# Kernel tuning notes

Measured on AMD Instinct MI355X. Metric: run time of the kernel, lower is better.

The kernel has to match this reference:

```python
import jax, jax.numpy as jnp
import numpy as np

DIM = 192
HEADS = 6
WS = (2, 7, 7)
SHIFT = (1, 3, 3)
MLP_HID = int(DIM * 4.0)
N = WS[0] * WS[1] * WS[2]  # 98


def _relative_position_index():
    wt, wh, ww = WS
    coords = np.stack(np.meshgrid(np.arange(wt), np.arange(wh), np.arange(ww), indexing='ij'))
    cf = coords.reshape(3, -1)  # (3, N)
    rel = cf[:, :, None] - cf[:, None, :]  # (3, N, N)
    rel = rel.transpose(1, 2, 0).copy()
    rel[:, :, 0] += wt - 1
    rel[:, :, 1] += wh - 1
    rel[:, :, 2] += ww - 1
    rel[:, :, 0] *= (2 * wh - 1) * (2 * ww - 1)
    rel[:, :, 1] *= 2 * ww - 1
    return rel.sum(-1)  # (N, N) int

RPI = jnp.asarray(_relative_position_index())


def setup_inputs() -> dict:
    key = jax.random.key(0)
    ks = jax.random.split(key, 12)
    B, C, T, H, W = 2, DIM, 8, 56, 56
    n_bias = (2 * WS[0] - 1) * (2 * WS[1] - 1) * (2 * WS[2] - 1)
    s = lambda k, shp, sd=0.02: jax.random.normal(k, shp, jnp.float32) * sd
    return {
        'x': jax.random.normal(ks[0], (B, C, T, H, W), jnp.float32),
        'mask_matrix': jnp.zeros((256, N, N), jnp.float32),
        'norm1_g': jnp.ones((DIM,), jnp.float32),
        'norm1_b': jnp.zeros((DIM,), jnp.float32),
        'qkv_w': s(ks[1], (DIM, 3 * DIM)),
        'qkv_b': jnp.zeros((3 * DIM,), jnp.float32),
        'proj_w': s(ks[2], (DIM, DIM)),
        'proj_b': jnp.zeros((DIM,), jnp.float32),
        'rpb_table': s(ks[3], (n_bias, HEADS)),
        'norm2_g': jnp.ones((DIM,), jnp.float32),
        'norm2_b': jnp.zeros((DIM,), jnp.float32),
        'fc1_w': s(ks[4], (DIM, MLP_HID)),
        'fc1_b': jnp.zeros((MLP_HID,), jnp.float32),
        'fc2_w': s(ks[5], (MLP_HID, DIM)),
        'fc2_b': jnp.zeros((DIM,), jnp.float32),
    }


def _layernorm(x, g, b, eps=1e-5):
    mu = jnp.mean(x, -1, keepdims=True)
    var = jnp.var(x, -1, keepdims=True)
    return (x - mu) * jax.lax.rsqrt(var + eps) * g + b


def _window_partition(x):
    # x: (B, T, H, W, C) -> (B*nW, N, C)
    B, T, H, W, C = x.shape
    wt, wh, ww = WS
    x = x.reshape(B, T // wt, wt, H // wh, wh, W // ww, ww, C)
    x = x.transpose(0, 1, 3, 5, 2, 4, 6, 7)
    return x.reshape(-1, wt * wh * ww, C)


def _window_reverse(win, B, T, H, W):
    wt, wh, ww = WS
    C = win.shape[-1]
    x = win.reshape(B, T // wt, H // wh, W // ww, wt, wh, ww, C)
    x = x.transpose(0, 1, 4, 2, 5, 3, 6, 7)
    return x.reshape(B, T, H, W, C)


def reference(x, mask_matrix, norm1_g, norm1_b, qkv_w, qkv_b, proj_w, proj_b,
              rpb_table, norm2_g, norm2_b, fc1_w, fc1_b, fc2_w, fc2_b):
    B, C, T, H, W = x.shape
    hd = C // HEADS
    scale = hd ** -0.5

    shortcut = x.transpose(0, 2, 3, 4, 1)  # (B,T,H,W,C) channel-last residual
    xn = _layernorm(shortcut, norm1_g, norm1_b)
    # cyclic shift
    xs = jnp.roll(xn, shift=(-SHIFT[0], -SHIFT[1], -SHIFT[2]), axis=(1, 2, 3))
    xw = _window_partition(xs)  # (B_, N, C)
    B_ = xw.shape[0]

    qkv = (xw @ qkv_w + qkv_b).reshape(B_, N, 3, HEADS, hd)
    q, k, v = (qkv[:, :, 0].transpose(0, 2, 1, 3),
               qkv[:, :, 1].transpose(0, 2, 1, 3),
               qkv[:, :, 2].transpose(0, 2, 1, 3))  # (B_, h, N, d)
    attn = jnp.einsum('bhnd,bhmd->bhnm', q * scale, k)
    bias = rpb_table[RPI.reshape(-1)].reshape(N, N, HEADS).transpose(2, 0, 1)
    attn = attn + bias[None]
    nW = mask_matrix.shape[0]
    attn = attn.reshape(B_ // nW, nW, HEADS, N, N) + mask_matrix[None, :, None]
    attn = jax.nn.softmax(attn.reshape(B_, HEADS, N, N), axis=-1)
    out = jnp.einsum('bhnm,bhmd->bhnd', attn, v).transpose(0, 2, 1, 3).reshape(B_, N, C)
    out = out @ proj_w + proj_b

    xr = _window_reverse(out, B, T, H, W)
    xr = jnp.roll(xr, shift=SHIFT, axis=(1, 2, 3))
    x1 = shortcut + xr

    xn2 = _layernorm(x1, norm2_g, norm2_b)
    h1 = jax.nn.gelu(xn2 @ fc1_w + fc1_b, approximate=False)
    x2 = x1 + (h1 @ fc2_w + fc2_b)
    return x2.transpose(0, 4, 1, 2, 3)  # (B, C, T, H, W)
```

## Files before the change

kernel.cpp:

```cpp
#include <hip/hip_runtime.h>
#include <hip/hip_bf16.h>
#include <math.h>

#define DEV __device__ __forceinline__

typedef __bf16 bf16;
typedef __bf16 bf16x8 __attribute__((ext_vector_type(8)));
typedef float f32x4 __attribute__((ext_vector_type(4)));

DEV f32x4 zero4() { f32x4 z; z[0]=0.f; z[1]=0.f; z[2]=0.f; z[3]=0.f; return z; }

DEV void gload_lds16(const bf16* g, bf16* l) {
    __builtin_amdgcn_global_load_lds(
        (const __attribute__((address_space(1))) void*)g,
        (__attribute__((address_space(3))) void*)l, 16, 0, 0);
}

DEV float gelu_f(float v) {
    float z = 0.7978845608028654f * (v + 0.044715f * v * v * v);
    float e = __expf(-2.0f * fabsf(z));
    float t = __builtin_copysignf((1.0f - e) / (1.0f + e), z);
    return 0.5f * v * (1.0f + t);
}


__global__ __launch_bounds__(256) void prep_w_k(
    const float* __restrict__ qw, const float* __restrict__ pw,
    const float* __restrict__ f1, const float* __restrict__ f2,
    bf16* __restrict__ qwt, bf16* __restrict__ pwt,
    bf16* __restrict__ f1t, bf16* __restrict__ f2t)
{
    int i = blockIdx.x * 256 + threadIdx.x;
    if (i < 576*192) { int n = i / 192, k = i % 192; qwt[i] = (bf16)qw[(size_t)k*576 + n]; }
    if (i < 192*192) { int n = i / 192, k = i % 192; pwt[i] = (bf16)pw[(size_t)k*192 + n]; }
    if (i < 768*192) { int n = i / 192, k = i % 192; f1t[i] = (bf16)f1[(size_t)k*768 + n]; }
    if (i < 192*768) { int n = i / 768, k = i % 768; f2t[i] = (bf16)f2[(size_t)k*192 + n]; }
}

__global__ __launch_bounds__(256) void prep_biasF_k(
    const float* __restrict__ rpb, float* __restrict__ biasF)
{
    int i = blockIdx.x * 256 + threadIdx.x;
    if (i >= 6*7*7*64) return;
    int lane = i & 63; int g = i >> 6;
    int j = g % 7; g /= 7; int rt = g % 7; int head = g / 7;
    int l15 = lane & 15, lg = lane >> 4;
    int nk = j*16 + l15;
    f32x4 o;
    #pragma unroll
    for (int r = 0; r < 4; r++) {
        int nq = rt*16 + lg*4 + r; if (nq > 97) nq = 97;
        if (nk < 98) {
            int t1 = nq/49, r1 = nq%49, h1 = r1/7, w1 = r1%7;
            int t2 = nk/49, r2 = nk%49, h2 = r2/7, w2 = r2%7;
            int idx = (t1 - t2 + 1)*169 + (h1 - h2 + 6)*13 + (w1 - w2 + 6);
            o[r] = rpb[idx*6 + head];
        } else {
            o[r] = -1e30f;
        }
    }
    *(f32x4*)&biasF[(size_t)i*4] = o;
}

__global__ __launch_bounds__(256) void prep_maskF_k(
    const float* __restrict__ maskm, float* __restrict__ maskF)
{
    int i = blockIdx.x * 256 + threadIdx.x;
    if (i >= 256*7*7*64) return;
    int lane = i & 63; int g = i >> 6;
    int j = g % 7; g /= 7; int rt = g % 7; int wib = g / 7;
    int l15 = lane & 15, lg = lane >> 4;
    int nk = j*16 + l15;
    f32x4 o;
    #pragma unroll
    for (int r = 0; r < 4; r++) {
        int nq = rt*16 + lg*4 + r; if (nq > 97) nq = 97;
        o[r] = (nk < 98) ? maskm[((size_t)wib*98 + nq)*98 + nk] : 0.f;
    }
    *(f32x4*)&maskF[(size_t)i*4] = o;
}

__global__ __launch_bounds__(256) void ln1_window_k(
    const float* __restrict__ x, const float* __restrict__ g,
    const float* __restrict__ bta, bf16* __restrict__ xw)
{
    __shared__ float tile[56*193];
    __shared__ float mu[56], rs[56];
    int blk = blockIdx.x;
    int bb = blk / 448; int r = blk % 448; int ts = r / 56; int hs = r % 56;
    int t = (ts + 1) & 7;
    int h = hs + 3; if (h >= 56) h -= 56;
    int tid = threadIdx.x;
    const float* xs = x + ((size_t)bb*1536 + t)*3136 + h*56;
    for (int e = tid; e < 192*56; e += 256) {
        int c = e / 56, w = e % 56;
        int wsp = w - 3; if (wsp < 0) wsp += 56;
        tile[wsp*193 + c] = xs[(size_t)c*25088 + w];
    }
    __syncthreads();
    if (tid < 224) {
        int row = tid >> 2, q = tid & 3;
        float s = 0.f, s2 = 0.f;
        for (int c = q*48; c < q*48 + 48; c++) {
            float v = tile[row*193 + c]; s += v; s2 += v*v;
        }
        s  += __shfl_xor(s, 1);  s  += __shfl_xor(s, 2);
        s2 += __shfl_xor(s2, 1); s2 += __shfl_xor(s2, 2);
        if (q == 0) {
            float m = s * (1.0f/192.0f);
            mu[row] = m;
            rs[row] = rsqrtf(s2 * (1.0f/192.0f) - m*m + 1e-5f);
        }
    }
    __syncthreads();
    int tb = ts >> 1, wt = ts & 1;
    int hb = hs / 7, wh = hs % 7;
    for (int e = tid; e < 56*192; e += 256) {
        int wpos = e / 192, c = e % 192;
        float v = (tile[wpos*193 + c] - mu[wpos]) * rs[wpos] * g[c] + bta[c];
        int wb = wpos / 7, ww = wpos % 7;
        int widx = bb*256 + tb*64 + hb*8 + wb;
        int n = wt*49 + wh*7 + ww;
        xw[((size_t)widx*98 + n)*192 + c] = (bf16)v;
    }
}

template<int KT, int NT, int BN, int EPI>
__global__ __launch_bounds__(256) void gemm_k(
    const bf16* __restrict__ A, const bf16* __restrict__ BT,
    const float* __restrict__ bias, const float* __restrict__ resid,
    void* __restrict__ outp)
{
    __shared__ bf16 la[2][128*64];
    __shared__ bf16 lb[2][BN*64];
    constexpr int NTILES = NT / BN;
    constexpr int NK = KT / 64;
    constexpr int JT = BN / 32;
    constexpr int WN = BN / 2;
    constexpr int SPX = 392 / 8;
    int blk = blockIdx.x;
    int xcd = blk & 7, ix = blk >> 3;
    int m0 = (xcd * SPX + ix / NTILES) * 128;
    int n0 = (ix % NTILES) * BN;
    int tid = threadIdx.x;
    int lane = tid & 63;
    int wv = tid >> 6;
    int wr = wv >> 1, wc = wv & 1;
    int l15 = lane & 15, lg = lane >> 4;

    auto stage = [&](int kt, int buf) {
        int kb = kt * 64;
        #pragma unroll
        for (int t = 0; t < 4; t++) {
            int e = t*256 + wv*64 + lane;
            int row = e >> 3, ck = e & 7;
            gload_lds16(&A[(size_t)(m0 + row)*KT + kb + ((ck ^ (row & 7)) << 3)],
                        &la[buf][(t*256 + wv*64) * 8]);
        }
        #pragma unroll
        for (int t = 0; t < JT; t++) {
            int e = t*256 + wv*64 + lane;
            int row = e >> 3, ck = e & 7;
            gload_lds16(&BT[(size_t)(n0 + row)*KT + kb + ((ck ^ (row & 7)) << 3)],
                        &lb[buf][(t*256 + wv*64) * 8]);
        }
    };

    f32x4 acc[4][JT];
    #pragma unroll
    for (int i = 0; i < 4; i++)
        #pragma unroll
        for (int j = 0; j < JT; j++) acc[i][j] = zero4();

    stage(0, 0);
    __syncthreads();

    for (int kt = 0; kt < NK; kt++) {
        int cur = kt & 1;
        if (kt + 1 < NK) stage(kt + 1, cur ^ 1);
        const bf16* lab = la[cur];
        const bf16* lbb = lb[cur];
        #pragma unroll
        for (int ks = 0; ks < 64; ks += 32) {
            int lc = (ks >> 3) + lg;
            bf16x8 af[4], bfr[JT];
            #pragma unroll
            for (int i = 0; i < 4; i++) {
                int ri = wr*64 + i*16 + l15;
                af[i] = *(const bf16x8*)&lab[ri*64 + ((lc ^ (ri & 7)) << 3)];
            }
            #pragma unroll
            for (int j = 0; j < JT; j++) {
                int rj = wc*WN + j*16 + l15;
                bfr[j] = *(const bf16x8*)&lbb[rj*64 + ((lc ^ (rj & 7)) << 3)];
            }
            #pragma unroll
            for (int i = 0; i < 4; i++)
                #pragma unroll
                for (int j = 0; j < JT; j++)
                    acc[i][j] = __builtin_amdgcn_mfma_f32_16x16x32_bf16(af[i], bfr[j], acc[i][j], 0, 0, 0);
        }
        __syncthreads();
    }

    if constexpr (EPI == 4) {
        #pragma unroll
        for (int i = 0; i < 4; i++) {
            #pragma unroll
            for (int j = 0; j < JT; j++) {
                int row0 = m0 + wr*64 + i*16 + lg*4;
                int col = n0 + wc*WN + j*16 + l15;
                f32x4 o;
                #pragma unroll
                for (int r = 0; r < 4; r++)
                    o[r] = acc[i][j][r] + bias[col] + resid[(size_t)(row0 + r)*NT + col];
                int bb2 = row0 >= 25088;
                size_t off = (size_t)bb2*192*25088 + (size_t)col*25088 + (row0 - bb2*25088);
                *(f32x4*)&((float*)outp)[off] = o;
            }
        }
    } else {
        #pragma unroll
        for (int i = 0; i < 4; i++) {
            #pragma unroll
            for (int j = 0; j < JT; j++) {
                #pragma unroll
                for (int r = 0; r < 4; r++) {
                    int row = m0 + wr*64 + i*16 + lg*4 + r;
                    int col = n0 + wc*WN + j*16 + l15;
                    float v = acc[i][j][r] + bias[col];
                    size_t oidx = (size_t)row * NT + col;
                    if constexpr (EPI == 0) {
                        ((bf16*)outp)[oidx] = (bf16)v;
                    } else if constexpr (EPI == 1) {
                        ((float*)outp)[oidx] = v;
                    } else if constexpr (EPI == 2) {
                        ((bf16*)outp)[oidx] = (bf16)gelu_f(v);
                    }
                }
            }
        }
    }
}

__global__ __launch_bounds__(128) void attn_k(
    const bf16* __restrict__ qkv, const float* __restrict__ biasF,
    const float* __restrict__ maskF, bf16* __restrict__ aout)
{
    __shared__ bf16 VT[32*128];
    __shared__ bf16 Pl[2*16*136];
    int blk = blockIdx.x;
    int t8 = (blk & 7) * 384 + (blk >> 3);
    int b_ = t8 / 6, head = t8 % 6;
    int tid = threadIdx.x, lane = tid & 63, wv = tid >> 6;
    int l15 = lane & 15, lg = (lane >> 4) & 3;
    int wib = b_ & 255;
    const bf16* base = qkv + (size_t)b_*98*576;

    {
        unsigned int* vz = (unsigned int*)VT;
        for (int e = tid; e < 2048; e += 128) vz[e] = 0u;
        unsigned int* pz = (unsigned int*)Pl;
        for (int e = tid; e < 256; e += 128) {
            int w2 = e >> 7, rem = e & 127;
            int row = rem >> 3, cp = rem & 7;
            pz[(w2*16 + row)*68 + 56 + cp] = 0u;
        }
    }
    __syncthreads();
    {
        int dq = tid >> 5;
        int kl = tid & 31;
        const bf16* vbase = base + 384 + head*32 + dq*8;
        #pragma unroll
        for (int kr = 0; kr < 4; kr++) {
            int k = kr*32 + kl;
            if (k < 98) {
                bf16x8 v8 = *(const bf16x8*)&vbase[(size_t)k*576];
                #pragma unroll
                for (int j = 0; j < 8; j++)
                    VT[(dq*8 + j)*128 + (k ^ (j << 3))] = v8[j];
            }
        }
    }
    __syncthreads();

    bf16x8 kfr[7];
    #pragma unroll
    for (int j = 0; j < 7; j++) {
        int krow = j*16 + l15; if (krow > 97) krow = 97;
        kfr[j] = *(const bf16x8*)&base[(size_t)krow*576 + 192 + head*32 + lg*8];
    }

    const float scale = 0.17677669529663687f;
    bf16* Pw = Pl + wv*16*136;
    const int rt0 = wv ? 4 : 0, rt1 = wv ? 7 : 4;

    auto loadQ = [&](int rt) {
        int qrow = rt*16 + l15; if (qrow > 97) qrow = 97;
        return *(const bf16x8*)&base[(size_t)qrow*576 + head*32 + lg*8];
    };
    bf16x8 qf = loadQ(rt0);

    #pragma unroll 1
    for (int rt = rt0; rt < rt1; rt++) {
        bf16x8 qnext = qf;
        if (rt + 1 < rt1) qnext = loadQ(rt + 1);
        f32x4 sacc[7];
        #pragma unroll
        for (int j = 0; j < 7; j++) sacc[j] = zero4();
        #pragma unroll
        for (int j = 0; j < 7; j++)
            sacc[j] = __builtin_amdgcn_mfma_f32_16x16x32_bf16(qf, kfr[j], sacc[j], 0, 0, 0);
        {
            const float* bfp = biasF + ((size_t)(head*7 + rt)*7)*256 + lane*4;
            const float* mfp = maskF + ((size_t)(wib*7 + rt)*7)*256 + lane*4;
            #pragma unroll
            for (int j = 0; j < 7; j++) {
                f32x4 bv = *(const f32x4*)&bfp[j*256];
                f32x4 mv = *(const f32x4*)&mfp[j*256];
                sacc[j] = sacc[j]*scale + bv + mv;
            }
            f32x4 m4 = sacc[0];
            #pragma unroll
            for (int j = 1; j < 7; j++) {
                #pragma unroll
                for (int r = 0; r < 4; r++) m4[r] = fmaxf(m4[r], sacc[j][r]);
            }
            #pragma unroll
            for (int d = 1; d < 16; d <<= 1) {
                #pragma unroll
                for (int r = 0; r < 4; r++) m4[r] = fmaxf(m4[r], __shfl_xor(m4[r], d));
            }
            f32x4 s4 = zero4();
            #pragma unroll
            for (int j = 0; j < 7; j++) {
                #pragma unroll
                for (int r = 0; r < 4; r++) sacc[j][r] = __expf(sacc[j][r] - m4[r]);
                s4 += sacc[j];
            }
            #pragma unroll
            for (int d = 1; d < 16; d <<= 1) {
                #pragma unroll
                for (int r = 0; r < 4; r++) s4[r] += __shfl_xor(s4[r], d);
            }
            f32x4 inv4;
            #pragma unroll
            for (int r = 0; r < 4; r++) inv4[r] = 1.0f / s4[r];
            #pragma unroll
            for (int j = 0; j < 7; j++)
                #pragma unroll
                for (int r = 0; r < 4; r++)
                    Pw[(lg*4 + r)*136 + j*16 + l15] = (bf16)(sacc[j][r]*inv4[r]);
        }
        #pragma unroll
        for (int dt = 0; dt < 2; dt++) {
            int dl = dt*16 + l15;
            int xr = (dl & 7) << 3;
            f32x4 oacc = zero4();
            #pragma unroll
            for (int kc = 0; kc < 4; kc++) {
                bf16x8 pf = *(const bf16x8*)&Pw[l15*136 + kc*32 + lg*8];
                bf16x8 vf = *(const bf16x8*)&VT[dl*128 + ((kc*32 + lg*8) ^ xr)];
                oacc = __builtin_amdgcn_mfma_f32_16x16x32_bf16(pf, vf, oacc, 0, 0, 0);
            }
            #pragma unroll
            for (int r = 0; r < 4; r++) {
                int row = rt*16 + lg*4 + r;
                if (row < 98)
                    aout[((size_t)b_*98 + row)*192 + head*32 + dt*16 + l15] = (bf16)oacc[r];
            }
        }
        qf = qnext;
    }
}

__global__ __launch_bounds__(256) void rev_res_ln2_k(
    const float* __restrict__ x, const float* __restrict__ pw,
    const float* __restrict__ g2, const float* __restrict__ b2,
    float* __restrict__ x1, bf16* __restrict__ xn2)
{
    __shared__ float tile[56*193];
    __shared__ float mu[56], rs[56];
    int blk = blockIdx.x;
    int bb = blk / 448; int r = blk % 448; int t = r / 56; int h = r % 56;
    int ts = (t + 7) & 7;
    int hs = h - 3; if (hs < 0) hs += 56;
    int tid = threadIdx.x;
    const float* xs = x + ((size_t)bb*1536 + t)*3136 + h*56;
    for (int e = tid; e < 192*56; e += 256) {
        int c = e / 56, w = e % 56;
        tile[w*193 + c] = xs[(size_t)c*25088 + w];
    }
    __syncthreads();
    int tb = ts >> 1, wt = ts & 1, hb = hs / 7, wh = hs % 7;
    for (int e = tid; e < 56*192; e += 256) {
        int w = e / 192, c = e % 192;
        int wsp = w - 3; if (wsp < 0) wsp += 56;
        int wb = wsp / 7, ww = wsp % 7;
        size_t tok = (size_t)(bb*256 + tb*64 + hb*8 + wb)*98 + wt*49 + wh*7 + ww;
        tile[w*193 + c] += pw[tok*192 + c];
    }
    __syncthreads();
    if (tid < 224) {
        int row = tid >> 2, q = tid & 3;
        float s = 0.f, s2 = 0.f;
        for (int c = q*48; c < q*48 + 48; c++) {
            float v = tile[row*193 + c]; s += v; s2 += v*v;
        }
        s  += __shfl_xor(s, 1);  s  += __shfl_xor(s, 2);
        s2 += __shfl_xor(s2, 1); s2 += __shfl_xor(s2, 2);
        if (q == 0) {
            float m = s * (1.0f/192.0f);
            mu[row] = m;
            rs[row] = rsqrtf(s2 * (1.0f/192.0f) - m*m + 1e-5f);
        }
    }
    __syncthreads();
    size_t tok0 = ((size_t)(bb*8 + t)*56 + h)*56;
    for (int e = tid; e < 56*192; e += 256) {
        int w = e / 192, c = e % 192;
        float v = tile[w*193 + c];
        x1[(tok0 + w)*192 + c] = v;
        xn2[(tok0 + w)*192 + c] = (bf16)((v - mu[w]) * rs[w] * g2[c] + b2[c]);
    }
}

extern "C" void kernel_launch(void* const* d_in, const int* in_sizes, int n_in,
                              void* d_out, int out_size, void* d_ws, size_t ws_size,
                              hipStream_t stream)
{
    const float* x     = (const float*)d_in[0];
    const float* maskm = (const float*)d_in[1];
    const float* n1g   = (const float*)d_in[2];
    const float* n1b   = (const float*)d_in[3];
    const float* qkvw  = (const float*)d_in[4];
    const float* qkvb  = (const float*)d_in[5];
    const float* projw = (const float*)d_in[6];
    const float* projb = (const float*)d_in[7];
    const float* rpb   = (const float*)d_in[8];
    const float* n2g   = (const float*)d_in[9];
    const float* n2b   = (const float*)d_in[10];
    const float* f1w   = (const float*)d_in[11];
    const float* f1b   = (const float*)d_in[12];
    const float* f2w   = (const float*)d_in[13];
    const float* f2b   = (const float*)d_in[14];

    char* ws = (char*)d_ws;
    bf16*  qkv_wt  = (bf16*)(ws + 0);
    bf16*  proj_wt = (bf16*)(ws + 221184);
    bf16*  fc1_wt  = (bf16*)(ws + 294912);
    bf16*  fc2_wt  = (bf16*)(ws + 589824);
    float* biasF   = (float*)(ws + 884736);
    bf16* xw   = (bf16*)(ws + 1179648);
    bf16* aout = xw;
    char* Bp = ws + 1179648 + 19267584;
    bf16*  qkv  = (bf16*)Bp;
    float* pwin = (float*)Bp;
    char* Cp = Bp + 57802752;
    float* x1  = (float*)Cp;
    bf16*  xn2 = (bf16*)(Cp + 38535168);
    bf16*  h1  = (bf16*)(Cp + 38535168 + 19267584);
    float* maskF = (float*)(Cp + 38535168 + 19267584);

    prep_w_k<<<576, 256, 0, stream>>>(qkvw, projw, f1w, f2w, qkv_wt, proj_wt, fc1_wt, fc2_wt);
    prep_biasF_k<<<74, 256, 0, stream>>>(rpb, biasF);
    prep_maskF_k<<<3136, 256, 0, stream>>>(maskm, maskF);
    ln1_window_k<<<896, 256, 0, stream>>>(x, n1g, n1b, xw);
    gemm_k<192, 576, 192, 0><<<392*3, 256, 0, stream>>>(xw, qkv_wt, qkvb, nullptr, qkv);
    attn_k<<<3072, 128, 0, stream>>>(qkv, biasF, maskF, aout);
    gemm_k<192, 192, 64, 1><<<392*3, 256, 0, stream>>>(aout, proj_wt, projb, nullptr, pwin);
    rev_res_ln2_k<<<896, 256, 0, stream>>>(x, pwin, n2g, n2b, x1, xn2);
    gemm_k<192, 768, 64, 2><<<392*12, 256, 0, stream>>>(xn2, fc1_wt, f1b, nullptr, h1);
    gemm_k<768, 192, 64, 4><<<392*3, 256, 0, stream>>>(h1, fc2_wt, f2b, x1, (float*)d_out);
}
```

Before: 237.0 us.

## Fuse fc1+GELU+fc2 MLP into one kernel keeping hidden activations in LDS

Measured after the change: 287.3 us. 1.21x slower.

```diff
diff --git a/kernel.cpp b/kernel.cpp
--- a/kernel.cpp
+++ b/kernel.cpp
@@ -19,8 +19,12 @@
 DEV float gelu_f(float v) {
     float z = 0.7978845608028654f * (v + 0.044715f * v * v * v);
     float e = __expf(-2.0f * fabsf(z));
-    float t = __builtin_copysignf((1.0f - e) / (1.0f + e), z);
+    float t = __builtin_copysignf((1.0f - e) * __builtin_amdgcn_rcpf(1.0f + e), z);
     return 0.5f * v * (1.0f + t);
+}
+
+DEV f32x4 bmfma(bf16x8 a, bf16x8 b, f32x4 c) {
+    return __builtin_amdgcn_mfma_f32_16x16x32_bf16(a, b, c, 0, 0, 0);
 }
 
 
@@ -198,47 +202,160 @@
             for (int i = 0; i < 4; i++)
                 #pragma unroll
                 for (int j = 0; j < JT; j++)
-                    acc[i][j] = __builtin_amdgcn_mfma_f32_16x16x32_bf16(af[i], bfr[j], acc[i][j], 0, 0, 0);
+                    acc[i][j] = bmfma(af[i], bfr[j], acc[i][j]);
         }
         __syncthreads();
     }
 
-    if constexpr (EPI == 4) {
-        #pragma unroll
-        for (int i = 0; i < 4; i++) {
-            #pragma unroll
-            for (int j = 0; j < JT; j++) {
-                int row0 = m0 + wr*64 + i*16 + lg*4;
+    #pragma unroll
+    for (int i = 0; i < 4; i++) {
+        #pragma unroll
+        for (int j = 0; j < JT; j++) {
+            #pragma unroll
+            for (int r = 0; r < 4; r++) {
+                int row = m0 + wr*64 + i*16 + lg*4 + r;
                 int col = n0 + wc*WN + j*16 + l15;
-                f32x4 o;
-                #pragma unroll
-                for (int r = 0; r < 4; r++)
-                    o[r] = acc[i][j][r] + bias[col] + resid[(size_t)(row0 + r)*NT + col];
-                int bb2 = row0 >= 25088;
-                size_t off = (size_t)bb2*192*25088 + (size_t)col*25088 + (row0 - bb2*25088);
-                *(f32x4*)&((float*)outp)[off] = o;
-            }
-        }
-    } else {
-        #pragma unroll
-        for (int i = 0; i < 4; i++) {
-            #pragma unroll
-            for (int j = 0; j < JT; j++) {
+                float v = acc[i][j][r] + bias[col];
+                size_t oidx = (size_t)row * NT + col;
+                if constexpr (EPI == 0) {
+                    ((bf16*)outp)[oidx] = (bf16)v;
+                } else if constexpr (EPI == 1) {
+                    ((float*)outp)[oidx] = v;
+                }
+            }
+        }
+    }
+}
+
+__global__ __launch_bounds__(256) void mlp_fused_k(
+    const bf16* __restrict__ xn2, const bf16* __restrict__ f1t,
+    const bf16* __restrict__ f2t, const float* __restrict__ f1b,
+    const float* __restrict__ f2b, const float* __restrict__ x1,
+    float* __restrict__ outp)
+{
+    __shared__ bf16 h1l[64*768];
+    __shared__ bf16 wb[2][192*64];
+    int blk = blockIdx.x;
+    int m0 = ((blk & 7) * 98 + (blk >> 3)) * 64;
+    int tid = threadIdx.x, lane = tid & 63, wv = tid >> 6;
+    int l15 = lane & 15, lg = lane >> 4;
+
+    auto stage1 = [&](int nc, int buf) {
+        #pragma unroll
+        for (int t = 0; t < 6; t++) {
+            int e = t*256 + tid;
+            int row = e / 24, ck = e % 24;
+            int sw = (ck & 24) | ((ck & 7) ^ (row & 7));
+            gload_lds16(&f1t[(size_t)(nc*64 + row)*192 + sw*8], &wb[buf][e*8]);
+        }
+    };
+    auto stage2 = [&](int kc, int buf) {
+        #pragma unroll
+        for (int t = 0; t < 6; t++) {
+            int e = t*256 + tid;
+            int row = e >> 3, ck = e & 7;
+            gload_lds16(&f2t[(size_t)row*768 + kc*64 + ((ck ^ (row & 7))*8)],
+                        &wb[buf][e*8]);
+        }
+    };
+
+    int rloc = (wv & 1) * 32;
+    int cloc = (wv >> 1) * 32;
+    bf16x8 af[2][6];
+    #pragma unroll
+    for (int rt = 0; rt < 2; rt++)
+        #pragma unroll
+        for (int kf = 0; kf < 6; kf++)
+            af[rt][kf] = *(const bf16x8*)&xn2[(size_t)(m0 + rloc + rt*16 + l15)*192 + kf*32 + lg*8];
+
+    stage1(0, 0);
+    __syncthreads();
+
+    for (int nc = 0; nc < 12; nc++) {
+        int buf = nc & 1;
+        if (nc < 11) stage1(nc + 1, buf ^ 1); else stage2(0, buf ^ 1);
+        f32x4 acc[2][2];
+        #pragma unroll
+        for (int a = 0; a < 2; a++)
+            #pragma unroll
+            for (int b = 0; b < 2; b++) acc[a][b] = zero4();
+        #pragma unroll
+        for (int ct = 0; ct < 2; ct++) {
+            int wrow = cloc + ct*16 + l15;
+            #pragma unroll
+            for (int kf = 0; kf < 6; kf++) {
+                int kcp = kf*4 + lg;
+                int phys = (kcp & 24) | ((kcp & 7) ^ (wrow & 7));
+                bf16x8 bfv = *(const bf16x8*)&wb[buf][wrow*192 + phys*8];
+                acc[0][ct] = bmfma(af[0][kf], bfv, acc[0][ct]);
+                acc[1][ct] = bmfma(af[1][kf], bfv, acc[1][ct]);
+            }
+        }
+        #pragma unroll
+        for (int rt = 0; rt < 2; rt++) {
+            #pragma unroll
+            for (int ct = 0; ct < 2; ct++) {
+                int col = nc*64 + cloc + ct*16 + l15;
+                float bv = f1b[col];
+                int kcw = col >> 3;
                 #pragma unroll
                 for (int r = 0; r < 4; r++) {
-                    int row = m0 + wr*64 + i*16 + lg*4 + r;
-                    int col = n0 + wc*WN + j*16 + l15;
-                    float v = acc[i][j][r] + bias[col];
-                    size_t oidx = (size_t)row * NT + col;
-                    if constexpr (EPI == 0) {
-                        ((bf16*)outp)[oidx] = (bf16)v;
-                    } else if constexpr (EPI == 1) {
-                        ((float*)outp)[oidx] = v;
-                    } else if constexpr (EPI == 2) {
-                        ((bf16*)outp)[oidx] = (bf16)gelu_f(v);
-                    }
+                    int row = rloc + rt*16 + lg*4 + r;
+                    float v = gelu_f(acc[rt][ct][r] + bv);
+                    int phys = (kcw & ~7) | ((kcw & 7) ^ (row & 7));
+                    h1l[row*768 + phys*8 + (l15 & 7)] = (bf16)v;
                 }
             }
+        }
+        __syncthreads();
+    }
+
+    f32x4 acc2[4][3];
+    #pragma unroll
+    for (int a = 0; a < 4; a++)
+        #pragma unroll
+        for (int b = 0; b < 3; b++) acc2[a][b] = zero4();
+    int ncol0 = wv * 48;
+    for (int kc = 0; kc < 12; kc++) {
+        int buf = kc & 1;
+        if (kc < 11) stage2(kc + 1, buf ^ 1);
+        #pragma unroll
+        for (int ks = 0; ks < 2; ks++) {
+            bf16x8 a2[4], b2[3];
+            #pragma unroll
+            for (int rt = 0; rt < 4; rt++) {
+                int row = rt*16 + l15;
+                int kcp = kc*8 + ks*4 + lg;
+                int phys = (kcp & ~7) | ((kcp & 7) ^ (row & 7));
+                a2[rt] = *(const bf16x8*)&h1l[row*768 + phys*8];
+            }
+            #pragma unroll
+            for (int nt = 0; nt < 3; nt++) {
+                int wrow = ncol0 + nt*16 + l15;
+                int ckr = ks*4 + lg;
+                b2[nt] = *(const bf16x8*)&wb[buf][wrow*64 + ((ckr ^ (wrow & 7))*8)];
+            }
+            #pragma unroll
+            for (int rt = 0; rt < 4; rt++)
+                #pragma unroll
+                for (int nt = 0; nt < 3; nt++)
+                    acc2[rt][nt] = bmfma(a2[rt], b2[nt], acc2[rt][nt]);
+        }
+        __syncthreads();
+    }
+    #pragma unroll
+    for (int rt = 0; rt < 4; rt++) {
+        #pragma unroll
+        for (int nt = 0; nt < 3; nt++) {
+            int row0 = m0 + rt*16 + lg*4;
+            int col = ncol0 + nt*16 + l15;
+            f32x4 o;
+            #pragma unroll
+            for (int r = 0; r < 4; r++)
+                o[r] = acc2[rt][nt][r] + f2b[col] + x1[(size_t)(row0 + r)*192 + col];
+            int bb2 = row0 >= 25088;
+            size_t off = (size_t)bb2*192*25088 + (size_t)col*25088 + (row0 - bb2*25088);
+            *(f32x4*)&outp[off] = o;
         }
     }
 }
@@ -311,7 +428,7 @@
         for (int j = 0; j < 7; j++) sacc[j] = zero4();
         #pragma unroll
         for (int j = 0; j < 7; j++)
-            sacc[j] = __builtin_amdgcn_mfma_f32_16x16x32_bf16(qf, kfr[j], sacc[j], 0, 0, 0);
+            sacc[j] = bmfma(qf, kfr[j], sacc[j]);
         {
             const float* bfp = biasF + ((size_t)(head*7 + rt)*7)*256 + lane*4;
             const float* mfp = maskF + ((size_t)(wib*7 + rt)*7)*256 + lane*4;
@@ -362,7 +479,7 @@
             for (int kc = 0; kc < 4; kc++) {
                 bf16x8 pf = *(const bf16x8*)&Pw[l15*136 + kc*32 + lg*8];
                 bf16x8 vf = *(const bf16x8*)&VT[dl*128 + ((kc*32 + lg*8) ^ xr)];
-                oacc = __builtin_amdgcn_mfma_f32_16x16x32_bf16(pf, vf, oacc, 0, 0, 0);
+                oacc = bmfma(pf, vf, oacc);
             }
             #pragma unroll
             for (int r = 0; r < 4; r++) {
@@ -460,7 +577,6 @@
     char* Cp = Bp + 57802752;
     float* x1  = (float*)Cp;
     bf16*  xn2 = (bf16*)(Cp + 38535168);
-    bf16*  h1  = (bf16*)(Cp + 38535168 + 19267584);
     float* maskF = (float*)(Cp + 38535168 + 19267584);
 
     prep_w_k<<<576, 256, 0, stream>>>(qkvw, projw, f1w, f2w, qkv_wt, proj_wt, fc1_wt, fc2_wt);
@@ -471,6 +587,5 @@
     attn_k<<<3072, 128, 0, stream>>>(qkv, biasF, maskF, aout);
     gemm_k<192, 192, 64, 1><<<392*3, 256, 0, stream>>>(aout, proj_wt, projb, nullptr, pwin);
     rev_res_ln2_k<<<896, 256, 0, stream>>>(x, pwin, n2g, n2b, x1, xn2);
-    gemm_k<192, 768, 64, 2><<<392*12, 256, 0, stream>>>(xn2, fc1_wt, f1b, nullptr, h1);
-    gemm_k<768, 192, 64, 4><<<392*3, 256, 0, stream>>>(h1, fc2_wt, f2b, x1, (float*)d_out);
-}
+    mlp_fused_k<<<784, 256, 0, stream>>>(xn2, fc1_wt, fc2_wt, f1b, f2b, x1, (float*)d_out);
+}
```
